# Kernel optimization log

Hardware: AMD Instinct MI355X
Metric: run time of the kernel (lower is better)

The kernel has to match this reference:

```python
import jax, jax.numpy as jnp
import numpy as np

# Model dims (match init_kwargs / input_specs)
L = 2      # layer_dim
B = 64     # batch
T = 512    # max seq len
D = 256    # input_dim (== hidden_dim, required by stacked wiring)
H = 256    # hidden_dim
O = 2      # output_dim


def setup_inputs() -> dict:
    key = jax.random.key(0)
    ks = jax.random.split(key, 10)
    s = 1.0 / np.sqrt(H)
    f32 = jnp.float32
    return {
        "x_data": jax.random.normal(ks[0], (B, T, D), f32),
        "x_length": jax.random.randint(ks[1], (B,), 1, T + 1),
        "x_label": jax.random.uniform(ks[2], (B,), f32),
        # Per-layer GRU-cell weights, stacked over layers (bias=False).
        "Wz": (jax.random.normal(ks[3], (L, D, H), f32) * s),
        "Uz": (jax.random.normal(ks[4], (L, H, H), f32) * s),
        "Wr": (jax.random.normal(ks[5], (L, D, H), f32) * s),
        "Ur": (jax.random.normal(ks[6], (L, H, H), f32) * s),
        "Wh": (jax.random.normal(ks[7], (L, D, H), f32) * s),
        "Uh": (jax.random.normal(ks[8], (L, H, H), f32) * s),
        # Output projection of the last layer (only last layer's `out` is used).
        "Wo": (jax.random.normal(ks[9], (H, O), f32) * s),
    }


def reference(x_data, x_length, x_label, Wz, Uz, Wr, Ur, Wh, Uh, Wo):
    # Training-mode forward: sum over batch and valid timesteps of
    # (label - sigmoid(out[:, 1]))**2, with per-layer states S1, S2
    # carried across time. Vectorized over batch; lax.scan over time.
    Tn = x_data.shape[1]
    xs = jnp.swapaxes(x_data, 0, 1)  # [T, B, D]
    S1_0 = jnp.zeros((L, B, H), x_data.dtype)
    S2_0 = jnp.zeros((L, B, H), x_data.dtype)

    def step(carry, xt):
        S1, S2 = carry
        inp = xt  # [B, D]
        for l in range(L):  # small fixed layer loop
            z = jax.nn.sigmoid(inp @ Wz[l] + S1[l] @ Uz[l])
            r = jax.nn.sigmoid(inp @ Wr[l] + S1[l] @ Ur[l])
            h = jnp.tanh(inp @ Wh[l] + (r * S1[l]) @ Uh[l])
            hn = (1.0 - z) * S1[l] + z * h          # new hidden (S1)
            S2n = z * S2[l] + (1.0 - z) * h          # secondary memory (S2)
            S1 = S1.at[l].set(hn)
            S2 = S2.at[l].set(S2n)
            inp = hn
        score = jax.nn.sigmoid((inp @ Wo)[:, 1])     # out[:, 1] -> [B]
        return (S1, S2), score

    _, scores = jax.lax.scan(step, (S1_0, S2_0), xs)  # [T, B]
    mask = (jnp.arange(Tn)[:, None] < x_length[None, :]).astype(scores.dtype)
    loss = jnp.sum(mask * (x_label[None, :] - scores) ** 2)
    return loss
```

## Files before the change

kernel.cpp:

```cpp
#include <hip/hip_runtime.h>

#define LAY 2
#define BATCH 64
#define TMAX 512
#define DIM 256
#define AST 264
#define CHUNK 16

typedef float floatx4 __attribute__((ext_vector_type(4)));
typedef __bf16 bf16x8 __attribute__((ext_vector_type(8)));
#define MFMA_FP8  __builtin_amdgcn_mfma_f32_16x16x32_fp8_fp8
#define MFMA_BF16 __builtin_amdgcn_mfma_f32_16x16x32_bf16

#define BAR_LDS() asm volatile("s_waitcnt lgkmcnt(0)\n\ts_barrier" ::: "memory")

#define OFF_WPW 0xA0000
#define OFF_FLG 0x150000
#define OFF_XP  0x200000
#define OFF_HP  0x1C00000
#define OFF_HN  0x3600000

__device__ __forceinline__ unsigned short f2bf(float f) {
    unsigned int u = __float_as_uint(f);
    unsigned int r = u + 0x7fffu + ((u >> 16) & 1u);
    return (unsigned short)(r >> 16);
}
__device__ __forceinline__ unsigned int pk2(float a, float b) {
    return (unsigned int)__builtin_amdgcn_cvt_pk_fp8_f32(a, b, 0, false);
}
__device__ __forceinline__ unsigned char f2q(float a) { return (unsigned char)(pk2(a, a) & 0xff); }
__device__ __forceinline__ void unp4(unsigned int u, float* f) {
    auto lo = __builtin_amdgcn_cvt_pk_f32_fp8((int)u, false);
    auto hi = __builtin_amdgcn_cvt_pk_f32_fp8((int)u, true);
    f[0] = lo[0]; f[1] = lo[1]; f[2] = hi[0]; f[3] = hi[1];
}
__device__ __forceinline__ float sigf(float x) {
    return __builtin_amdgcn_rcpf(1.f + __expf(-x));
}
__device__ __forceinline__ float tanhfast2y(float twoy) { return 2.f * sigf(twoy) - 1.f; }

__device__ __forceinline__ void ast_u32(unsigned int* p, unsigned int v) {
    __hip_atomic_store(p, v, __ATOMIC_RELAXED, __HIP_MEMORY_SCOPE_AGENT);
}

__device__ __forceinline__ long quant8(const float* s) {
    unsigned int p01 = pk2(8.f * s[0 * 256], 8.f * s[1 * 256]);
    unsigned int p23 = pk2(8.f * s[2 * 256], 8.f * s[3 * 256]);
    unsigned int p45 = pk2(8.f * s[4 * 256], 8.f * s[5 * 256]);
    unsigned int p67 = pk2(8.f * s[6 * 256], 8.f * s[7 * 256]);
    unsigned long long v = (unsigned long long)(p01 & 0xffffu)
                         | ((unsigned long long)(p23 & 0xffffu) << 16)
                         | ((unsigned long long)(p45 & 0xffffu) << 32)
                         | ((unsigned long long)(p67 & 0xffffu) << 48);
    return (long)v;
}

__global__ void prep_weights(const float* __restrict__ Wz, const float* __restrict__ Wr,
                             const float* __restrict__ Wh,
                             unsigned char* __restrict__ ws, float* __restrict__ out) {
    int T = blockIdx.x * 256 + threadIdx.x;
    if (T == 0) out[0] = 0.f;
    if (T < 192) ((int*)(ws + OFF_FLG))[T] = 0;
    int e = T & 3, lane = (T >> 2) & 63;
    int kf = (T >> 8) & 7, nt = (T >> 11) & 15, mw = T >> 15;
    const float* s = (mw == 0 ? Wz : mw == 1 ? Wr : Wh);
    int n  = nt * 16 + (lane & 15);
    int k0 = kf * 32 + (lane >> 4) * 8 + 2 * e;
    unsigned int v = (unsigned int)f2bf(s[(k0 << 8) + n]) |
                     ((unsigned int)f2bf(s[((k0 + 1) << 8) + n]) << 16);
    int addr = ((mw * 16 + nt) * 8 + kf) * 1024 + lane * 16 + 4 * e;
    *(unsigned int*)(ws + OFF_WPW + addr) = v;
}

template <int SCORE, int WMODE, int POST>
__device__ __forceinline__ void scan_body(
    const unsigned int* __restrict__ xp,
    const float* __restrict__ Uzs, const float* __restrict__ Urs,
    const float* __restrict__ Uhs,
    int bg, unsigned char* __restrict__ hnout,
    const int* __restrict__ xlen, const float* __restrict__ xlab,
    const float* __restrict__ Wo, float* __restrict__ out,
    int* wflags, int* pflag,
    unsigned char (*s1q)[AST], unsigned char (*rsq)[AST], float (*s1o)[264],
    float* wo1s, int* s_rdy, int tmax)
{
    const int tid = threadIdx.x, wave = tid >> 6, lane = tid & 63;
    const int l15 = lane & 15, quad = lane >> 4;
    const int b0 = bg * 16;

    for (int i = tid; i < 16 * AST; i += 1024) ((unsigned char*)s1q)[i] = 0;
    if (SCORE && tid < DIM) wo1s[tid] = Wo[2 * tid + 1];
    const int lenr = xlen[b0 + l15];
    const float labr = SCORE ? xlab[b0 + l15] : 0.f;
    (void)lenr; (void)labr;

    const int nt = wave;
    const int colA = nt * 16 + l15, rowb = quad * 4;

    long uz[8], ur[8], uh[8];
    {
        const int nb = nt * 16 + l15;
#pragma unroll
        for (int kf = 0; kf < 8; ++kf) {
            const size_t kb = (size_t)(kf * 32 + quad * 8) * 256 + nb;
            uz[kf] = quant8(Uzs + kb);
            ur[kf] = quant8(Urs + kb);
            uh[kf] = quant8(Uhs + kb);
        }
    }
    float s1r[4] = {};
    float accl = 0.f;
    int ready = 0;
    __syncthreads();

    for (int t = 0; t < tmax; ++t) {
        if constexpr (WMODE == 1) {
            if (t >= ready) {
                if (tid == 0) {
                    int vv, g = 0;
                    for (;;) {
                        vv = 1 << 30;
#pragma unroll
                        for (int q = 0; q < 4; ++q) {
                            int m = __hip_atomic_load(wflags + q, __ATOMIC_RELAXED, __HIP_MEMORY_SCOPE_AGENT);
                            vv = m < vv ? m : vv;
                        }
                        if (vv > t || ++g > (1 << 19)) break;
                        __builtin_amdgcn_s_sleep(2);
                    }
                    __threadfence();
                    *s_rdy = vv > t ? vv : t + 1;
                }
                __syncthreads();
                ready = *s_rdy;
            }
        } else if constexpr (WMODE == 2) {
            if (t >= ready) {
                if (tid == 0) {
                    const int ch = t >> 4;
                    int g = 0;
                    for (;;) {
                        int c = __hip_atomic_load(wflags + ch, __ATOMIC_RELAXED, __HIP_MEMORY_SCOPE_AGENT);
                        if (c >= 16 || ++g > (1 << 19)) break;
                        __builtin_amdgcn_s_sleep(2);
                    }
                    __threadfence();
                    *s_rdy = (ch + 1) * CHUNK;
                }
                __syncthreads();
                ready = *s_rdy;
            }
        }

        const unsigned int* xpt = xp + ((size_t)(bg * 512 + t) * 1024 + nt * 64 + lane) * 3;
        unsigned int xz = xpt[0];
        unsigned int xr = xpt[1];
        unsigned int xh = xpt[2];

        long sf[8];
#pragma unroll
        for (int kf = 0; kf < 8; ++kf) sf[kf] = *(const long*)&s1q[l15][kf * 32 + quad * 8];
        floatx4 za = {0.f, 0.f, 0.f, 0.f}, ra = za;
#pragma unroll
        for (int kf = 0; kf < 8; ++kf) {
            ra = MFMA_FP8(sf[kf], ur[kf], ra, 0, 0, 0);
            za = MFMA_FP8(sf[kf], uz[kf], za, 0, 0, 0);
        }
        float xrf[4];
        unp4(xr, xrf);
#pragma unroll
        for (int i = 0; i < 4; ++i) {
            float r = sigf(0.125f * ra[i] + 0.0625f * xrf[i]);
            rsq[rowb + i][colA] = f2q(r * s1r[i]);
        }
        BAR_LDS();

        long rf[8];
#pragma unroll
        for (int kf = 0; kf < 8; ++kf) rf[kf] = *(const long*)&rsq[l15][kf * 32 + quad * 8];
        floatx4 ha = {0.f, 0.f, 0.f, 0.f};
#pragma unroll
        for (int kf = 0; kf < 8; ++kf) ha = MFMA_FP8(rf[kf], uh[kf], ha, 0, 0, 0);
        float xzf[4], xhf[4];
        unp4(xz, xzf); unp4(xh, xhf);
#pragma unroll
        for (int i = 0; i < 4; ++i) {
            float z = sigf(0.125f * za[i] + 0.0625f * xzf[i]);
            float h = tanhfast2y(0.25f * ha[i] + 0.125f * xhf[i]);
            float hn = fmaf(z, h - s1r[i], s1r[i]);
            s1r[i] = hn;
            s1q[rowb + i][colA] = f2q(hn);
            if (SCORE) s1o[rowb + i][colA] = hn;
        }
        BAR_LDS();

        if (!SCORE) {
            const int r = tid >> 6, c = (tid & 63) * 4;
            unsigned int v4 = *(const unsigned int*)&s1q[r][c];
            *(unsigned int*)(hnout + ((size_t)(b0 + r) * 512 + t) * 256 + c) = v4;
        } else if (wave == 0) {
            const int row = l15, c0 = quad * 64;
            float p = 0.f;
#pragma unroll
            for (int u = 0; u < 64; u += 4) {
                float4 sv = *(const float4*)&s1o[row][c0 + u];
                float4 wv = *(const float4*)&wo1s[c0 + u];
                p = fmaf(sv.x, wv.x, p); p = fmaf(sv.y, wv.y, p);
                p = fmaf(sv.z, wv.z, p); p = fmaf(sv.w, wv.w, p);
            }
            p += __shfl_xor(p, 16);
            p += __shfl_xor(p, 32);
            if (lane < 16 && t < lenr) {
                float sc = sigf(p);
                float d = labr - sc;
                accl = fmaf(d, d, accl);
            }
        }

        if (POST && (((t & (CHUNK - 1)) == (CHUNK - 1)) || t == tmax - 1)) {
            __syncthreads();
            if (tid == 0) {
                __threadfence();
                __hip_atomic_store(pflag, t + 1, __ATOMIC_RELEASE, __HIP_MEMORY_SCOPE_AGENT);
            }
        }
    }

    if (SCORE && wave == 0) {
        accl += __shfl_xor(accl, 1);
        accl += __shfl_xor(accl, 2);
        accl += __shfl_xor(accl, 4);
        accl += __shfl_xor(accl, 8);
        if (lane == 0) atomicAdd(out, accl);
    }
}

__global__ __launch_bounds__(1024, 4) void fused_pipeline(
    const float* __restrict__ x,
    unsigned int* __restrict__ XP, unsigned int* __restrict__ HP,
    const unsigned char* __restrict__ wpW, unsigned char* __restrict__ HN,
    const int* __restrict__ xlen, const float* __restrict__ xlab,
    const float* __restrict__ Wo, float* __restrict__ out, int* flags,
    const float* __restrict__ Uz, const float* __restrict__ Ur,
    const float* __restrict__ Uh,
    const float* __restrict__ Wz, const float* __restrict__ Wr,
    const float* __restrict__ Wh)
{
    __shared__ __align__(16) unsigned char s1q[16][AST];
    __shared__ __align__(16) unsigned char rsq[16][AST];
    __shared__ __align__(16) float s1o[16][264];
    __shared__ float wo1s[DIM];
    __shared__ int s_rdy;

    const int bid = blockIdx.x;
    const int tid = threadIdx.x, wave = tid >> 6, lane = tid & 63;
    const int l15 = lane & 15, quad = lane >> 4;
    int* cnt = flags + 32;

    if (bid >= 24) {
        const int idx = bid - 24;
        const int pt = idx & 511, pbg = idx >> 9;
        const float* s = x + ((size_t)(pbg * 16 + l15) * 512 + pt) * 256;
        bf16x8 af[8];
#pragma unroll
        for (int kf = 0; kf < 8; ++kf) {
            float4 a = *(const float4*)(s + kf * 32 + quad * 8);
            float4 b = *(const float4*)(s + kf * 32 + quad * 8 + 4);
            union { unsigned short u[8]; bf16x8 v; } cv;
            cv.u[0] = f2bf(a.x); cv.u[1] = f2bf(a.y); cv.u[2] = f2bf(a.z); cv.u[3] = f2bf(a.w);
            cv.u[4] = f2bf(b.x); cv.u[5] = f2bf(b.y); cv.u[6] = f2bf(b.z); cv.u[7] = f2bf(b.w);
            af[kf] = cv.v;
        }
        floatx4 az = {0.f, 0.f, 0.f, 0.f}, ar = az, ah = az;
        const unsigned char* bz = wpW + (size_t)((0 * 16 + wave) * 8) * 1024 + lane * 16;
        const unsigned char* br = wpW + (size_t)((1 * 16 + wave) * 8) * 1024 + lane * 16;
        const unsigned char* bh = wpW + (size_t)((2 * 16 + wave) * 8) * 1024 + lane * 16;
#pragma unroll
        for (int kf = 0; kf < 8; ++kf) {
            az = MFMA_BF16(af[kf], *(const bf16x8*)(bz + kf * 1024), az, 0, 0, 0);
            ar = MFMA_BF16(af[kf], *(const bf16x8*)(br + kf * 1024), ar, 0, 0, 0);
            ah = MFMA_BF16(af[kf], *(const bf16x8*)(bh + kf * 1024), ah, 0, 0, 0);
        }
        const size_t ob3 = ((size_t)(pbg * 512 + pt) * 1024 + wave * 64 + lane) * 3;
        ast_u32(&XP[ob3 + 0], pk2(16.f * az[0], 16.f * az[1]) | (pk2(16.f * az[2], 16.f * az[3]) << 16));
        ast_u32(&XP[ob3 + 1], pk2(16.f * ar[0], 16.f * ar[1]) | (pk2(16.f * ar[2], 16.f * ar[3]) << 16));
        ast_u32(&XP[ob3 + 2], pk2(16.f * ah[0], 16.f * ah[1]) | (pk2(16.f * ah[2], 16.f * ah[3]) << 16));
        __syncthreads();
        if (tid == 0)
            __hip_atomic_fetch_add(cnt + pbg * 32 + (pt >> 4), 1,
                                   __ATOMIC_RELAXED, __HIP_MEMORY_SCOPE_AGENT);
        return;
    }

    int role, bg, p = 0;
    if (bid < 4)       { role = 0; bg = bid; }
    else if (bid < 20) { role = 1; bg = (bid - 4) >> 2; p = (bid - 4) & 3; }
    else               { role = 2; bg = bid - 20; }
    const int b0 = bg * 16;

    int v = xlen[b0 + l15];
#pragma unroll
    for (int o = 1; o < 16; o <<= 1) v = max(v, __shfl_xor(v, o));
    const int tmax = __builtin_amdgcn_readfirstlane(v);

    if (role == 0) {
        scan_body<0, 2, 1>(XP, Uz, Ur, Uh, bg, HN, xlen, xlab, Wo, out,
                           cnt + bg * 32, flags + bg, s1q, rsq, s1o, wo1s, &s_rdy, tmax);
    } else if (role == 2) {
        scan_body<1, 1, 0>(HP, Uz + 65536, Ur + 65536, Uh + 65536, bg, nullptr,
                           xlen, xlab, Wo, out,
                           flags + 4 + bg * 4, nullptr, s1q, rsq, s1o, wo1s, &s_rdy, tmax);
    } else {
        int* wf = flags + bg;
        int* pf = flags + 4 + bg * 4 + p;
        const int nt = wave;
        long wz1[8], wr1[8], wh1[8];
        {
            const int nb = nt * 16 + l15;
#pragma unroll
            for (int kf = 0; kf < 8; ++kf) {
                const size_t kb = (size_t)(kf * 32 + quad * 8) * 256 + nb;
                wz1[kf] = quant8(Wz + 65536 + kb);
                wr1[kf] = quant8(Wr + 65536 + kb);
                wh1[kf] = quant8(Wh + 65536 + kb);
            }
        }
        for (int base = 0; base < tmax; base += CHUNK) {
            const int target = (base + CHUNK < tmax) ? base + CHUNK : tmax;
            if (tid == 0) {
                int vv, g = 0;
                for (;;) {
                    vv = __hip_atomic_load(wf, __ATOMIC_RELAXED, __HIP_MEMORY_SCOPE_AGENT);
                    if (vv >= target || ++g > (1 << 19)) break;
                    __builtin_amdgcn_s_sleep(2);
                }
                __threadfence();
            }
            __syncthreads();

            const int t0 = base + p * 4;
            const int t1 = (t0 + 4 < tmax) ? t0 + 4 : tmax;
            for (int t = t0; t < t1; ++t) {
                const unsigned char* sA = HN + ((size_t)(b0 + l15) * 512 + t) * 256;
                long af[8];
#pragma unroll
                for (int kf = 0; kf < 8; ++kf) af[kf] = *(const long*)(sA + kf * 32 + quad * 8);
                floatx4 az = {0.f, 0.f, 0.f, 0.f}, ar = az, ah = az;
#pragma unroll
                for (int kf = 0; kf < 8; ++kf) {
                    az = MFMA_FP8(af[kf], wz1[kf], az, 0, 0, 0);
                    ar = MFMA_FP8(af[kf], wr1[kf], ar, 0, 0, 0);
                    ah = MFMA_FP8(af[kf], wh1[kf], ah, 0, 0, 0);
                }
                const size_t ob3 = ((size_t)(bg * 512 + t) * 1024 + nt * 64 + lane) * 3;
                HP[ob3 + 0] = pk2(2.f * az[0], 2.f * az[1]) | (pk2(2.f * az[2], 2.f * az[3]) << 16);
                HP[ob3 + 1] = pk2(2.f * ar[0], 2.f * ar[1]) | (pk2(2.f * ar[2], 2.f * ar[3]) << 16);
                HP[ob3 + 2] = pk2(2.f * ah[0], 2.f * ah[1]) | (pk2(2.f * ah[2], 2.f * ah[3]) << 16);
            }

            __syncthreads();
            if (tid == 0) {
                __threadfence();
                __hip_atomic_store(pf, base + CHUNK, __ATOMIC_RELEASE, __HIP_MEMORY_SCOPE_AGENT);
            }
        }
    }
}

extern "C" void kernel_launch(void* const* d_in, const int* in_sizes, int n_in,
                              void* d_out, int out_size, void* d_ws, size_t ws_size,
                              hipStream_t stream) {
    const float* x    = (const float*)d_in[0];
    const int*   xlen = (const int*)d_in[1];
    const float* xlab = (const float*)d_in[2];
    const float* Wz   = (const float*)d_in[3];
    const float* Uz   = (const float*)d_in[4];
    const float* Wr   = (const float*)d_in[5];
    const float* Ur   = (const float*)d_in[6];
    const float* Wh   = (const float*)d_in[7];
    const float* Uh   = (const float*)d_in[8];
    const float* Wo   = (const float*)d_in[9];
    float* out = (float*)d_out;

    unsigned char* ws  = (unsigned char*)d_ws;
    unsigned char* wpW = ws + OFF_WPW;
    int*           FLG = (int*)(ws + OFF_FLG);
    unsigned int*  XP  = (unsigned int*)(ws + OFF_XP);
    unsigned int*  HP  = (unsigned int*)(ws + OFF_HP);
    unsigned char* HN  = ws + OFF_HN;

    prep_weights<<<384, 256, 0, stream>>>(Wz, Wr, Wh, ws, out);
    fused_pipeline<<<2072, 1024, 0, stream>>>(x, XP, HP, wpW, HN,
                                              xlen, xlab, Wo, out, FLG,
                                              Uz, Ur, Uh, Wz, Wr, Wh);
}
```

Baseline: 1.126 ms.

## Split MFMA accumulator chains, coalesce XP stores via LDS, skip ahead on ready chunks

The recurrent step's FP8 MFMA reductions are split into two independent accumulator chains per gate and summed at the end, which shortens the dependent MFMA latency chain on the serial critical path. The projection blocks stage their packed outputs in shared memory so the global stores become contiguous per thread instead of stride-3. The consumer wait loop also scans forward over chunks that are already complete, so it polls flags less often. In exchange there is an extra barrier and about 12 KB of extra LDS per block, which may affect occupancy, plus a small change in summation order.

```diff
diff --git a/kernel.cpp b/kernel.cpp
--- a/kernel.cpp
+++ b/kernel.cpp
@@ -144,8 +144,12 @@
                         if (c >= 16 || ++g > (1 << 19)) break;
                         __builtin_amdgcn_s_sleep(2);
                     }
+                    int ch2 = ch + 1;
+                    while (ch2 < TMAX / CHUNK &&
+                           __hip_atomic_load(wflags + ch2, __ATOMIC_RELAXED,
+                                             __HIP_MEMORY_SCOPE_AGENT) >= 16) ++ch2;
                     __threadfence();
-                    *s_rdy = (ch + 1) * CHUNK;
+                    *s_rdy = ch2 * CHUNK;
                 }
                 __syncthreads();
                 ready = *s_rdy;
@@ -160,12 +164,16 @@
         long sf[8];
 #pragma unroll
         for (int kf = 0; kf < 8; ++kf) sf[kf] = *(const long*)&s1q[l15][kf * 32 + quad * 8];
-        floatx4 za = {0.f, 0.f, 0.f, 0.f}, ra = za;
-#pragma unroll
-        for (int kf = 0; kf < 8; ++kf) {
-            ra = MFMA_FP8(sf[kf], ur[kf], ra, 0, 0, 0);
-            za = MFMA_FP8(sf[kf], uz[kf], za, 0, 0, 0);
-        }
+        floatx4 zer = {0.f, 0.f, 0.f, 0.f};
+        floatx4 ra0 = zer, ra1 = zer, za0 = zer, za1 = zer;
+#pragma unroll
+        for (int kf = 0; kf < 4; ++kf) {
+            ra0 = MFMA_FP8(sf[kf],     ur[kf],     ra0, 0, 0, 0);
+            ra1 = MFMA_FP8(sf[kf + 4], ur[kf + 4], ra1, 0, 0, 0);
+            za0 = MFMA_FP8(sf[kf],     uz[kf],     za0, 0, 0, 0);
+            za1 = MFMA_FP8(sf[kf + 4], uz[kf + 4], za1, 0, 0, 0);
+        }
+        floatx4 ra = ra0 + ra1;
         float xrf[4];
         unp4(xr, xrf);
 #pragma unroll
@@ -178,9 +186,14 @@
         long rf[8];
 #pragma unroll
         for (int kf = 0; kf < 8; ++kf) rf[kf] = *(const long*)&rsq[l15][kf * 32 + quad * 8];
-        floatx4 ha = {0.f, 0.f, 0.f, 0.f};
-#pragma unroll
-        for (int kf = 0; kf < 8; ++kf) ha = MFMA_FP8(rf[kf], uh[kf], ha, 0, 0, 0);
+        floatx4 ha0 = zer, ha1 = zer;
+#pragma unroll
+        for (int kf = 0; kf < 4; ++kf) {
+            ha0 = MFMA_FP8(rf[kf],     uh[kf],     ha0, 0, 0, 0);
+            ha1 = MFMA_FP8(rf[kf + 4], uh[kf + 4], ha1, 0, 0, 0);
+        }
+        floatx4 ha = ha0 + ha1;
+        floatx4 za = za0 + za1;
         float xzf[4], xhf[4];
         unp4(xz, xzf); unp4(xh, xhf);
 #pragma unroll
@@ -251,6 +264,7 @@
     __shared__ __align__(16) float s1o[16][264];
     __shared__ float wo1s[DIM];
     __shared__ int s_rdy;
+    __shared__ __align__(16) unsigned int xpstage[3072];
 
     const int bid = blockIdx.x;
     const int tid = threadIdx.x, wave = tid >> 6, lane = tid & 63;
@@ -281,10 +295,14 @@
             ar = MFMA_BF16(af[kf], *(const bf16x8*)(br + kf * 1024), ar, 0, 0, 0);
             ah = MFMA_BF16(af[kf], *(const bf16x8*)(bh + kf * 1024), ah, 0, 0, 0);
         }
-        const size_t ob3 = ((size_t)(pbg * 512 + pt) * 1024 + wave * 64 + lane) * 3;
-        ast_u32(&XP[ob3 + 0], pk2(16.f * az[0], 16.f * az[1]) | (pk2(16.f * az[2], 16.f * az[3]) << 16));
-        ast_u32(&XP[ob3 + 1], pk2(16.f * ar[0], 16.f * ar[1]) | (pk2(16.f * ar[2], 16.f * ar[3]) << 16));
-        ast_u32(&XP[ob3 + 2], pk2(16.f * ah[0], 16.f * ah[1]) | (pk2(16.f * ah[2], 16.f * ah[3]) << 16));
+        xpstage[tid * 3 + 0] = pk2(16.f * az[0], 16.f * az[1]) | (pk2(16.f * az[2], 16.f * az[3]) << 16);
+        xpstage[tid * 3 + 1] = pk2(16.f * ar[0], 16.f * ar[1]) | (pk2(16.f * ar[2], 16.f * ar[3]) << 16);
+        xpstage[tid * 3 + 2] = pk2(16.f * ah[0], 16.f * ah[1]) | (pk2(16.f * ah[2], 16.f * ah[3]) << 16);
+        __syncthreads();
+        const size_t base3 = (size_t)(pbg * 512 + pt) * 3072;
+        ast_u32(&XP[base3 + tid],        xpstage[tid]);
+        ast_u32(&XP[base3 + 1024 + tid], xpstage[1024 + tid]);
+        ast_u32(&XP[base3 + 2048 + tid], xpstage[2048 + tid]);
         __syncthreads();
         if (tid == 0)
             __hip_atomic_fetch_add(cnt + pbg * 32 + (pt >> 4), 1,
```

New measurement: 1.081 ms (median of 2 runs). -4.0%, faster.
